# Performance work log

Measured on AMD Instinct MI355X. Metric: run time of the kernel, lower is better.

Reference implementation:

```python
import jax, jax.numpy as jnp
import numpy as np
from jax.scipy.ndimage import map_coordinates

H = 256          # detector height (pixels)
W = 256          # detector width (pixels)
PX = 1.6875      # pixel size (mm); W*PX = 432mm
PIERCE = 216.0   # piercing point offset (mm) -> centered detector
SAD = 742.5      # source-to-isocenter distance (mm)
DAD = 517.15     # detector-to-isocenter distance (mm)


def _rotmat(angles):
    # ZYX intrinsic Euler rotation from (alpha, beta, gamma)
    a, b, g = angles[0], angles[1], angles[2]
    ca, sa = jnp.cos(a), jnp.sin(a)
    cb, sb = jnp.cos(b), jnp.sin(b)
    cg, sg = jnp.cos(g), jnp.sin(g)
    Rz = jnp.array([[ca, -sa, 0.], [sa, ca, 0.], [0., 0., 1.]])
    Ry = jnp.array([[cb, 0., sb], [0., 1., 0.], [-sb, 0., cb]])
    Rx = jnp.array([[1., 0., 0.], [0., cg, -sg], [0., sg, cg]])
    return Rz @ Ry @ Rx


def setup_inputs() -> dict:
    key = jax.random.key(0)
    k1, k2 = jax.random.split(key)
    volume = jax.random.uniform(k1, (256, 256, 256), dtype=jnp.float32)  # CT attenuation
    batch = jax.random.normal(k2, (2, 6), dtype=jnp.float32) * 0.1       # [B, (rot3, trans3)]
    return {"volume": volume, "batch": batch, "n_samples": 256}


def reference(volume, batch, n_samples):
    B = batch.shape[0]
    center = jnp.asarray(volume.shape, dtype=volume.dtype) / 2.0  # volume center (mm, unit spacing)

    rots = batch[:, 0:3]
    trans = batch[:, 3:6]
    R = jax.vmap(_rotmat)(rots)                              # [B,3,3]
    iso = center[None, :] + trans                            # [B,3]

    z = jnp.array([0., 0., 1.], dtype=volume.dtype)
    source = iso + SAD * jnp.einsum('bij,j->bi', R, z)       # [B,3]
    det_c = iso - DAD * jnp.einsum('bij,j->bi', R, z)        # [B,3]
    u_ax = R[:, :, 0]                                        # detector u axis [B,3]
    v_ax = R[:, :, 1]                                        # detector v axis [B,3]

    us = (jnp.arange(W, dtype=volume.dtype) * PX - PIERCE)   # [W]
    vs = (jnp.arange(H, dtype=volume.dtype) * PX - PIERCE)   # [H]
    # target pixel positions on detector plane: [B,H,W,3]
    target = (det_c[:, None, None, :]
              + us[None, None, :, None] * u_ax[:, None, None, :]
              + vs[None, :, None, None] * v_ax[:, None, None, :])

    ray = target - source[:, None, None, :]                  # [B,H,W,3]
    length = jnp.linalg.norm(ray, axis=-1)                   # [B,H,W]

    t = jnp.linspace(0.0, 1.0, n_samples, dtype=volume.dtype)  # [S]
    # sample points along each ray: [B,S,H,W,3] (voxel coords, unit spacing)
    pts = source[:, None, None, None, :] + t[None, :, None, None, None] * ray[:, None, :, :, :]

    def sample_one(p):  # p: [S,H,W,3]
        return map_coordinates(volume, [p[..., 0], p[..., 1], p[..., 2]], order=1, mode='constant', cval=0.0)

    samples = jax.vmap(sample_one)(pts)                      # [B,S,H,W]
    img = samples.sum(axis=1) * (length / n_samples)         # line integral [B,H,W]

    img = img.reshape(B, -1)                                 # [B, H*W]
    mn = img.min(axis=1, keepdims=True)
    mx = img.max(axis=1, keepdims=True)
    img = (img - mn) / (mx - mn)
    img = 1.0 - img                                          # bone_dark=True
    return img.reshape(B, H, W)
```

## Files before the change

kernel.cpp:

```cpp
#include <hip/hip_runtime.h>
#include <hip/hip_fp16.h>


static __device__ __constant__ float kPX     = 1.6875f;
static __device__ __constant__ float kPIERCE = 216.0f;
static __device__ __constant__ float kSAD    = 742.5f;
static __device__ __constant__ float kDAD    = 517.15f;

#define VOL_BYTES   (256u * 256u * 256u * 4u)
#define PAIR_R      258u
#define PAIR_ELEMS  (256u * 256u * PAIR_R)
#define PAIR_BYTES  (PAIR_ELEMS * 4u)

__global__ void drr_init_mm(unsigned* mm) {
    int i = threadIdx.x;
    if (i < 4) mm[i] = (i & 1) ? 0u : 0x7F800000u;
}

__global__ __launch_bounds__(256) void drr_pack(const float* __restrict__ vol,
                                                __half2* __restrict__ vhp,
                                                unsigned* __restrict__ mm) {
    if (blockIdx.x == 0 && threadIdx.x < 4)
        mm[threadIdx.x] = (threadIdx.x & 1) ? 0u : 0x7F800000u;

    __shared__ float tile[65][65];
    const int bid  = blockIdx.x;
    const int y    = bid >> 4;
    const int t4   = bid & 15;
    const int x0   = (t4 & 3) << 6;
    const int z0   = (t4 >> 2) << 6;

    const int rr = threadIdx.x >> 4;
    const int cc = threadIdx.x & 15;
    #pragma unroll
    for (int base = 0; base < 80; base += 16) {
        const int r = base + rr;
        if (r < 65) {
            const int x = x0 - 1 + r;
            float4 f = make_float4(0.0f, 0.0f, 0.0f, 0.0f);
            if (x >= 0)
                f = *(const float4*)&vol[(x << 16) | (y << 8) | (z0 + (cc << 2))];
            tile[r][(cc << 2) + 0] = f.x;
            tile[r][(cc << 2) + 1] = f.y;
            tile[r][(cc << 2) + 2] = f.z;
            tile[r][(cc << 2) + 3] = f.w;
        }
    }
    __syncthreads();

    const int lane = threadIdx.x & 63;
    const int row4 = threadIdx.x >> 6;
    for (int r = row4; r < 64; r += 4) {
        const int z = z0 + r;
        const unsigned base = (unsigned)((z << 8) | y) * PAIR_R;
        vhp[base + x0 + lane] =
            __halves2half2(__float2half(tile[lane][r]), __float2half(tile[lane + 1][r]));
    }
    if ((t4 & 3) == 3) {
        for (int r = row4; r < 64; r += 4) {
            const int z = z0 + r;
            const unsigned base = (unsigned)((z << 8) | y) * PAIR_R;
            if (lane == 0) {
                vhp[base + 256] = __halves2half2(__float2half(tile[64][r]), __float2half(0.0f));
                vhp[base + 257] = __halves2half2(__float2half(0.0f), __float2half(0.0f));
            }
        }
    }
}

__device__ __forceinline__ void slab(float s, float r, float lo, float hi,
                                     float& tlo, float& thi) {
    if (fabsf(r) > 1e-8f) {
        const float inv = 1.0f / r;
        const float ta  = (lo - s) * inv;
        const float tb  = (hi - s) * inv;
        tlo = fmaxf(tlo, fminf(ta, tb));
        thi = fminf(thi, fmaxf(ta, tb));
    } else if (s < lo || s > hi) {
        tlo = 2.0f; thi = -1.0f;
    }
}

struct RayCfg {
    float rx, ry, rz, length;
    int k_lo, k_hi;
    int s_lo, s_hi;
};

__device__ __forceinline__ void cfg_windows(float sx, float sy, float sz, RayCfg& c) {
    float tlo = 0.0f, thi = 1.0f;
    slab(sx, c.rx, -1.02f, 256.02f, tlo, thi);
    slab(sy, c.ry, -1.02f, 256.02f, tlo, thi);
    slab(sz, c.rz, -1.02f, 256.02f, tlo, thi);
    c.k_lo = 0; c.k_hi = -1;
    if (thi >= tlo) {
        c.k_lo = max(0,   (int)ceilf(tlo * 255.0f - 1e-3f));
        c.k_hi = min(255, (int)floorf(thi * 255.0f + 1e-3f));
    }
    float slo = 0.0f, shi = 1.0f;
    slab(sx, c.rx, 0.01f, 254.99f, slo, shi);
    slab(sy, c.ry, 0.01f, 254.99f, slo, shi);
    slab(sz, c.rz, 0.01f, 254.99f, slo, shi);
    c.s_lo = 1; c.s_hi = -1;
    if (shi >= slo) {
        c.s_lo = (int)ceilf(slo * 255.0f + 1e-3f);
        c.s_hi = (int)floorf(shi * 255.0f - 1e-3f);
    }
}

__device__ __forceinline__ void ray_setup2(const float* __restrict__ batch,
                                           int b, int u, int v0,
                                           float& sx, float& sy, float& sz,
                                           RayCfg& A, RayCfg& B) {
    const float a  = batch[b * 6 + 0];
    const float be = batch[b * 6 + 1];
    const float g  = batch[b * 6 + 2];
    const float tx = batch[b * 6 + 3];
    const float ty = batch[b * 6 + 4];
    const float tz = batch[b * 6 + 5];

    float sa, ca, sb, cb, sg, cg;
    sincosf(a, &sa, &ca);
    sincosf(be, &sb, &cb);
    sincosf(g, &sg, &cg);

    const float R00 = ca * cb;
    const float R01 = ca * sb * sg - sa * cg;
    const float R02 = sa * sg + ca * sb * cg;
    const float R10 = sa * cb;
    const float R11 = ca * cg + sa * sb * sg;
    const float R12 = sa * sb * cg - ca * sg;
    const float R20 = -sb;
    const float R21 = cb * sg;
    const float R22 = cb * cg;

    sx = 128.0f + tx + kSAD * R02;
    sy = 128.0f + ty + kSAD * R12;
    sz = 128.0f + tz + kSAD * R22;

    const float uu = u * kPX - kPIERCE;
    const float vv = v0 * kPX - kPIERCE;
    A.rx = uu * R00 + vv * R01 - (kSAD + kDAD) * R02;
    A.ry = uu * R10 + vv * R11 - (kSAD + kDAD) * R12;
    A.rz = uu * R20 + vv * R21 - (kSAD + kDAD) * R22;
    B.rx = A.rx + kPX * R01;
    B.ry = A.ry + kPX * R11;
    B.rz = A.rz + kPX * R21;
    A.length = sqrtf(A.rx * A.rx + A.ry * A.ry + A.rz * A.rz);
    B.length = sqrtf(B.rx * B.rx + B.ry * B.ry + B.rz * B.rz);
    cfg_windows(sx, sy, sz, A);
    cfg_windows(sx, sy, sz, B);
}

__device__ __forceinline__ float tri_fast(const __half2* __restrict__ vhp,
                                          float sx, float sy, float sz,
                                          const RayCfg& c, float t) {
    const float px = fmaf(t, c.rx, sx);
    const float py = fmaf(t, c.ry, sy);
    const float pz = fmaf(t, c.rz, sz);
    const float fx = floorf(px), fy = floorf(py), fz = floorf(pz);
    const int ix = (int)fx, iy = (int)fy, iz = (int)fz;
    const float wx = px - fx, wy = py - fy, wz = pz - fz;

    const unsigned base = (unsigned)iz * 66048u + (unsigned)iy * 258u + (unsigned)(ix + 1);
    const __half2 q00 = vhp[base];
    const __half2 q01 = vhp[base + 66048u];
    const __half2 q10 = vhp[base + 258u];
    const __half2 q11 = vhp[base + 66306u];

    const float wx0 = 1.0f - wx, wy0 = 1.0f - wy, wz0 = 1.0f - wz;
    const float a00 = __low2float(q00) * wx0 + __high2float(q00) * wx;
    const float a01 = __low2float(q01) * wx0 + __high2float(q01) * wx;
    const float a10 = __low2float(q10) * wx0 + __high2float(q10) * wx;
    const float a11 = __low2float(q11) * wx0 + __high2float(q11) * wx;
    return (a00 * wz0 + a01 * wz) * wy0 + (a10 * wz0 + a11 * wz) * wy;
}

__device__ __forceinline__ float tri_slow(const __half2* __restrict__ vhp,
                                          float sx, float sy, float sz,
                                          const RayCfg& c, float t) {
    const float px = fmaf(t, c.rx, sx);
    const float py = fmaf(t, c.ry, sy);
    const float pz = fmaf(t, c.rz, sz);
    const float fx = floorf(px), fy = floorf(py), fz = floorf(pz);
    const int ix = (int)fx, iy = (int)fy, iz = (int)fz;
    const float wx = px - fx, wy = py - fy, wz = pz - fz;

    const float mx0 = ((unsigned)ix       < 256u) ? 1.0f : 0.0f;
    const float mx1 = ((unsigned)(ix + 1) < 256u) ? 1.0f : 0.0f;
    const float my0 = ((unsigned)iy       < 256u) ? 1.0f : 0.0f;
    const float my1 = ((unsigned)(iy + 1) < 256u) ? 1.0f : 0.0f;
    const float mz0 = ((unsigned)iz       < 256u) ? 1.0f : 0.0f;
    const float mz1 = ((unsigned)(iz + 1) < 256u) ? 1.0f : 0.0f;

    const int i  = min(max(ix + 1, 0), 257);
    const int y0 = min(max(iy,     0), 255);
    const int y1 = min(max(iy + 1, 0), 255);
    const int z0 = min(max(iz,     0), 255);
    const int z1 = min(max(iz + 1, 0), 255);

    const unsigned zt0 = (unsigned)z0 * 66048u;
    const unsigned zt1 = (unsigned)z1 * 66048u;
    const unsigned yt0 = (unsigned)y0 * 258u;
    const unsigned yt1 = (unsigned)y1 * 258u;

    const __half2 q00 = vhp[zt0 + yt0 + i];
    const __half2 q01 = vhp[zt1 + yt0 + i];
    const __half2 q10 = vhp[zt0 + yt1 + i];
    const __half2 q11 = vhp[zt1 + yt1 + i];

    const float wx0 = (1.0f - wx) * mx0, wx1 = wx * mx1;
    const float wy0 = (1.0f - wy) * my0, wy1 = wy * my1;
    const float wz0 = (1.0f - wz) * mz0, wz1 = wz * mz1;

    const float a00 = __low2float(q00) * wx0 + __high2float(q00) * wx1;
    const float a01 = __low2float(q01) * wx0 + __high2float(q01) * wx1;
    const float a10 = __low2float(q10) * wx0 + __high2float(q10) * wx1;
    const float a11 = __low2float(q11) * wx0 + __high2float(q11) * wx1;
    return (a00 * wz0 + a01 * wz1) * wy0 + (a10 * wz0 + a11 * wz1) * wy1;
}

__global__ __launch_bounds__(512, 4) void drr_main_pk2(const __half2* __restrict__ vhp,
                                                       const float* __restrict__ batch,
                                                       float* __restrict__ raw,
                                                       unsigned* __restrict__ mm) {
    const int tid  = threadIdx.x;
    const int lane = tid & 63;
    const int seg  = tid >> 6;

    const int blk = ((blockIdx.x & 7) << 7) | (blockIdx.x >> 3);
    const int b   = blk >> 9;
    const int ti  = blk & 511;
    const int u   = ((ti & 15) << 4) + (lane & 15);
    const int v0  = ((ti >> 4) << 3) + ((lane >> 4) << 1);

    float sx, sy, sz;
    RayCfg A, B;
    ray_setup2(batch, b, u, v0, sx, sy, sz, A, B);

    const int klo = min(A.k_lo, B.k_lo);
    const int khi = max(A.k_hi, B.k_hi);
    const int slo = max(A.s_lo, B.s_lo);
    const int shi = min(A.s_hi, B.s_hi);

    const float tstep = 1.0f / 255.0f;
    float sA = 0.0f, sB = 0.0f;
    for (int k = klo + seg; k <= khi; k += 8) {
        const float t = (float)k * tstep;
        if (k >= slo && k <= shi) {
            sA += tri_fast(vhp, sx, sy, sz, A, t);
            sB += tri_fast(vhp, sx, sy, sz, B, t);
        } else {
            sA += tri_slow(vhp, sx, sy, sz, A, t);
            sB += tri_slow(vhp, sx, sy, sz, B, t);
        }
    }

    __shared__ float pA[8][64], pB[8][64];
    pA[seg][lane] = sA;
    pB[seg][lane] = sB;
    __syncthreads();

    if (tid < 64) {
        float tA = 0.0f, tB = 0.0f;
        #pragma unroll
        for (int s = 0; s < 8; ++s) { tA += pA[s][lane]; tB += pB[s][lane]; }
        const float rA = tA * (A.length * (1.0f / 256.0f));
        const float rB = tB * (B.length * (1.0f / 256.0f));
        raw[(b << 16) + (v0 << 8) + u]       = rA;
        raw[(b << 16) + ((v0 + 1) << 8) + u] = rB;

        float mn = fminf(rA, rB), mx = fmaxf(rA, rB);
        #pragma unroll
        for (int off = 32; off >= 1; off >>= 1) {
            mn = fminf(mn, __shfl_xor(mn, off));
            mx = fmaxf(mx, __shfl_xor(mx, off));
        }
        if (lane == 0) {
            atomicMin(&mm[2 * b + 0], __float_as_uint(mn));
            atomicMax(&mm[2 * b + 1], __float_as_uint(mx));
        }
    }
}

__global__ __launch_bounds__(256) void drr_transpose(const float* __restrict__ vol,
                                                     float* __restrict__ volt) {
    __shared__ float tile[64][65];
    const int bid  = blockIdx.x;
    const int y    = bid >> 4;
    const int t4   = bid & 15;
    const int x0   = (t4 & 3) << 6;
    const int z0   = (t4 >> 2) << 6;
    const int lane = threadIdx.x & 63;
    const int row4 = threadIdx.x >> 6;

    #pragma unroll
    for (int i = 0; i < 16; ++i) {
        const int xr = (i << 2) + row4;
        tile[xr][lane] = vol[((x0 + xr) << 16) | (y << 8) | (z0 + lane)];
    }
    __syncthreads();
    #pragma unroll
    for (int i = 0; i < 16; ++i) {
        const int zr = (i << 2) + row4;
        volt[((z0 + zr) << 16) | (y << 8) | (x0 + lane)] = tile[lane][zr];
    }
}

__device__ __forceinline__ float tri_sample_f32(const float* __restrict__ vol,
                                                float sx, float sy, float sz,
                                                const RayCfg& c, float t) {
    const float px = fmaf(t, c.rx, sx);
    const float py = fmaf(t, c.ry, sy);
    const float pz = fmaf(t, c.rz, sz);
    const float fx = floorf(px), fy = floorf(py), fz = floorf(pz);
    const int ix = (int)fx, iy = (int)fy, iz = (int)fz;
    const float wx = px - fx, wy = py - fy, wz = pz - fz;
    const float mx0 = ((unsigned)ix       < 256u) ? 1.0f : 0.0f;
    const float mx1 = ((unsigned)(ix + 1) < 256u) ? 1.0f : 0.0f;
    const float my0 = ((unsigned)iy       < 256u) ? 1.0f : 0.0f;
    const float my1 = ((unsigned)(iy + 1) < 256u) ? 1.0f : 0.0f;
    const float mz0 = ((unsigned)iz       < 256u) ? 1.0f : 0.0f;
    const float mz1 = ((unsigned)(iz + 1) < 256u) ? 1.0f : 0.0f;
    const unsigned X0 = (unsigned)ix & 255u, X1 = (unsigned)(ix + 1) & 255u;
    const unsigned Y0 = ((unsigned)iy & 255u) << 8, Y1 = ((unsigned)(iy + 1) & 255u) << 8;
    const unsigned Z0 = ((unsigned)iz & 255u) << 16, Z1 = ((unsigned)(iz + 1) & 255u) << 16;
    const float v000 = vol[Z0 | Y0 | X0];
    const float v001 = vol[Z1 | Y0 | X0];
    const float v010 = vol[Z0 | Y1 | X0];
    const float v011 = vol[Z1 | Y1 | X0];
    const float v100 = vol[Z0 | Y0 | X1];
    const float v101 = vol[Z1 | Y0 | X1];
    const float v110 = vol[Z0 | Y1 | X1];
    const float v111 = vol[Z1 | Y1 | X1];
    const float wx0 = (1.0f - wx) * mx0, wx1 = wx * mx1;
    const float wy0 = (1.0f - wy) * my0, wy1 = wy * my1;
    const float wz0 = (1.0f - wz) * mz0, wz1 = wz * mz1;
    const float c00 = v000 * wz0 + v001 * wz1;
    const float c01 = v010 * wz0 + v011 * wz1;
    const float c10 = v100 * wz0 + v101 * wz1;
    const float c11 = v110 * wz0 + v111 * wz1;
    return (c00 * wy0 + c01 * wy1) * wx0 + (c10 * wy0 + c11 * wy1) * wx1;
}

__global__ __launch_bounds__(256, 4) void drr_main_f32(const float* __restrict__ volt,
                                                       const float* __restrict__ batch,
                                                       float* __restrict__ raw,
                                                       unsigned* __restrict__ mm) {
    const int tid  = threadIdx.x;
    const int lane = tid & 63;
    const int seg  = tid >> 6;
    const int tile = blockIdx.x;
    const int b    = tile >> 10;
    const int ti   = tile & 1023;
    const int u    = ((ti & 15) << 4) + (lane & 15);
    const int v    = ((ti >> 4) << 2) + (lane >> 4);

    float sx, sy, sz;
    RayCfg A, B;
    ray_setup2(batch, b, u, v, sx, sy, sz, A, B);

    const float tstep = 1.0f / 255.0f;
    float sum = 0.0f;
    for (int k = A.k_lo + seg; k <= A.k_hi; k += 4)
        sum += tri_sample_f32(volt, sx, sy, sz, A, (float)k * tstep);

    __shared__ float part[4][64];
    part[seg][lane] = sum;
    __syncthreads();

    if (tid < 64) {
        const float s = part[0][lane] + part[1][lane] + part[2][lane] + part[3][lane];
        const float rawv = s * (A.length * (1.0f / 256.0f));
        raw[(b << 16) + (v << 8) + u] = rawv;
        float mn = rawv, mx = rawv;
        #pragma unroll
        for (int off = 32; off >= 1; off >>= 1) {
            mn = fminf(mn, __shfl_xor(mn, off));
            mx = fmaxf(mx, __shfl_xor(mx, off));
        }
        if (lane == 0) {
            atomicMin(&mm[2 * b + 0], __float_as_uint(mn));
            atomicMax(&mm[2 * b + 1], __float_as_uint(mx));
        }
    }
}

__global__ __launch_bounds__(256) void drr_norm(float* __restrict__ img,
                                                const unsigned* __restrict__ mm) {
    const int gid = blockIdx.x * 256 + threadIdx.x;
    const int b   = gid >> 16;
    const float mn  = __uint_as_float(mm[2 * b + 0]);
    const float mx  = __uint_as_float(mm[2 * b + 1]);
    const float inv = 1.0f / (mx - mn);
    img[gid] = 1.0f - (img[gid] - mn) * inv;
}

extern "C" void kernel_launch(void* const* d_in, const int* in_sizes, int n_in,
                              void* d_out, int out_size, void* d_ws, size_t ws_size,
                              hipStream_t stream) {
    const float* vol   = (const float*)d_in[0];
    const float* batch = (const float*)d_in[1];
    float* out         = (float*)d_out;

    if (ws_size >= (size_t)PAIR_BYTES + 16) {
        __half2*  vhp = (__half2*)d_ws;
        unsigned* mm  = (unsigned*)((char*)d_ws + PAIR_BYTES);
        drr_pack<<<4096, 256, 0, stream>>>(vol, vhp, mm);
        drr_main_pk2<<<1024, 512, 0, stream>>>(vhp, batch, out, mm);
        drr_norm<<<512, 256, 0, stream>>>(out, mm);
    } else {
        float*    volt = (float*)d_ws;
        unsigned* mm   = (unsigned*)((char*)d_ws + VOL_BYTES);
        drr_init_mm<<<1, 64, 0, stream>>>(mm);
        drr_transpose<<<4096, 256, 0, stream>>>(vol, volt);
        drr_main_f32<<<2048, 256, 0, stream>>>(volt, batch, out, mm);
        drr_norm<<<512, 256, 0, stream>>>(out, mm);
    }
}
```

Measured before the change: 95.13 us.

## Split ray samples across four blocks with atomic accumulation and separate min/max pass

The main ray-marching kernel now splits each tile's sample range across four 256-thread blocks (4096 blocks in total) instead of one 512-thread block per tile. Partial line integrals are combined with float atomicAdd into an output that the pack kernel zeroes first. Because per-pixel sums are only final once all blocks finish, the min/max reduction moves into a new kernel launched before normalisation. The half-precision pack also switches to a packed round-toward-zero conversion intrinsic. In exchange this adds atomics, an extra launch and nondeterministic summation order.

```diff
diff --git a/kernel.cpp b/kernel.cpp
--- a/kernel.cpp
+++ b/kernel.cpp
@@ -12,6 +12,13 @@
 #define PAIR_ELEMS  (256u * 256u * PAIR_R)
 #define PAIR_BYTES  (PAIR_ELEMS * 4u)
 
+typedef __fp16 half2_raw __attribute__((ext_vector_type(2)));
+
+__device__ __forceinline__ __half2 pack_h2(float lo, float hi) {
+    half2_raw h = __builtin_amdgcn_cvt_pkrtz(lo, hi);
+    return __builtin_bit_cast(__half2, h);
+}
+
 __global__ void drr_init_mm(unsigned* mm) {
     int i = threadIdx.x;
     if (i < 4) mm[i] = (i & 1) ? 0u : 0x7F800000u;
@@ -19,12 +26,15 @@
 
 __global__ __launch_bounds__(256) void drr_pack(const float* __restrict__ vol,
                                                 __half2* __restrict__ vhp,
+                                                float* __restrict__ raw,
                                                 unsigned* __restrict__ mm) {
-    if (blockIdx.x == 0 && threadIdx.x < 4)
+    const int bid = blockIdx.x;
+    if (bid == 0 && threadIdx.x < 4)
         mm[threadIdx.x] = (threadIdx.x & 1) ? 0u : 0x7F800000u;
+    if (threadIdx.x < 32)
+        raw[(bid << 5) + threadIdx.x] = 0.0f;
 
     __shared__ float tile[65][65];
-    const int bid  = blockIdx.x;
     const int y    = bid >> 4;
     const int t4   = bid & 15;
     const int x0   = (t4 & 3) << 6;
@@ -53,16 +63,15 @@
     for (int r = row4; r < 64; r += 4) {
         const int z = z0 + r;
         const unsigned base = (unsigned)((z << 8) | y) * PAIR_R;
-        vhp[base + x0 + lane] =
-            __halves2half2(__float2half(tile[lane][r]), __float2half(tile[lane + 1][r]));
+        vhp[base + x0 + lane] = pack_h2(tile[lane][r], tile[lane + 1][r]);
     }
     if ((t4 & 3) == 3) {
         for (int r = row4; r < 64; r += 4) {
             const int z = z0 + r;
             const unsigned base = (unsigned)((z << 8) | y) * PAIR_R;
             if (lane == 0) {
-                vhp[base + 256] = __halves2half2(__float2half(tile[64][r]), __float2half(0.0f));
-                vhp[base + 257] = __halves2half2(__float2half(0.0f), __float2half(0.0f));
+                vhp[base + 256] = pack_h2(tile[64][r], 0.0f);
+                vhp[base + 257] = pack_h2(0.0f, 0.0f);
             }
         }
     }
@@ -220,19 +229,19 @@
     return (a00 * wz0 + a01 * wz1) * wy0 + (a10 * wz0 + a11 * wz1) * wy1;
 }
 
-__global__ __launch_bounds__(512, 4) void drr_main_pk2(const __half2* __restrict__ vhp,
+__global__ __launch_bounds__(256, 8) void drr_main_pk3(const __half2* __restrict__ vhp,
                                                        const float* __restrict__ batch,
-                                                       float* __restrict__ raw,
-                                                       unsigned* __restrict__ mm) {
+                                                       float* __restrict__ raw) {
     const int tid  = threadIdx.x;
     const int lane = tid & 63;
     const int seg  = tid >> 6;
 
-    const int blk = ((blockIdx.x & 7) << 7) | (blockIdx.x >> 3);
-    const int b   = blk >> 9;
-    const int ti  = blk & 511;
-    const int u   = ((ti & 15) << 4) + (lane & 15);
-    const int v0  = ((ti >> 4) << 3) + ((lane >> 4) << 1);
+    const int kq   = blockIdx.x & 3;
+    const int tile = blockIdx.x >> 2;
+    const int b    = tile >> 9;
+    const int ti   = tile & 511;
+    const int u    = ((ti & 15) << 4) + (lane & 15);
+    const int v0   = ((ti >> 4) << 3) + ((lane >> 4) << 1);
 
     float sx, sy, sz;
     RayCfg A, B;
@@ -245,7 +254,7 @@
 
     const float tstep = 1.0f / 255.0f;
     float sA = 0.0f, sB = 0.0f;
-    for (int k = klo + seg; k <= khi; k += 8) {
+    for (int k = klo + (kq << 2) + seg; k <= khi; k += 16) {
         const float t = (float)k * tstep;
         if (k >= slo && k <= shi) {
             sA += tri_fast(vhp, sx, sy, sz, A, t);
@@ -256,31 +265,46 @@
         }
     }
 
-    __shared__ float pA[8][64], pB[8][64];
+    __shared__ float pA[4][64], pB[4][64];
     pA[seg][lane] = sA;
     pB[seg][lane] = sB;
     __syncthreads();
 
     if (tid < 64) {
-        float tA = 0.0f, tB = 0.0f;
-        #pragma unroll
-        for (int s = 0; s < 8; ++s) { tA += pA[s][lane]; tB += pB[s][lane]; }
-        const float rA = tA * (A.length * (1.0f / 256.0f));
-        const float rB = tB * (B.length * (1.0f / 256.0f));
-        raw[(b << 16) + (v0 << 8) + u]       = rA;
-        raw[(b << 16) + ((v0 + 1) << 8) + u] = rB;
-
-        float mn = fminf(rA, rB), mx = fmaxf(rA, rB);
-        #pragma unroll
-        for (int off = 32; off >= 1; off >>= 1) {
-            mn = fminf(mn, __shfl_xor(mn, off));
-            mx = fmaxf(mx, __shfl_xor(mx, off));
-        }
-        if (lane == 0) {
-            atomicMin(&mm[2 * b + 0], __float_as_uint(mn));
-            atomicMax(&mm[2 * b + 1], __float_as_uint(mx));
-        }
-    }
+        const float tA = pA[0][lane] + pA[1][lane] + pA[2][lane] + pA[3][lane];
+        const float tB = pB[0][lane] + pB[1][lane] + pB[2][lane] + pB[3][lane];
+        if (tA != 0.0f)
+            atomicAdd(&raw[(b << 16) + (v0 << 8) + u],       tA * (A.length * (1.0f / 256.0f)));
+        if (tB != 0.0f)
+            atomicAdd(&raw[(b << 16) + ((v0 + 1) << 8) + u], tB * (B.length * (1.0f / 256.0f)));
+    }
+}
+
+__global__ __launch_bounds__(256) void drr_minmax(const float* __restrict__ raw,
+                                                  unsigned* __restrict__ mm) {
+    const int gid = blockIdx.x * 256 + threadIdx.x;
+    const int b   = gid >> 16;
+    const float x = raw[gid];
+    float mn = x, mx = x;
+    #pragma unroll
+    for (int off = 32; off >= 1; off >>= 1) {
+        mn = fminf(mn, __shfl_xor(mn, off));
+        mx = fmaxf(mx, __shfl_xor(mx, off));
+    }
+    if ((threadIdx.x & 63) == 0) {
+        atomicMin(&mm[2 * b + 0], __float_as_uint(mn));
+        atomicMax(&mm[2 * b + 1], __float_as_uint(mx));
+    }
+}
+
+__global__ __launch_bounds__(256) void drr_norm(float* __restrict__ img,
+                                                const unsigned* __restrict__ mm) {
+    const int gid = blockIdx.x * 256 + threadIdx.x;
+    const int b   = gid >> 16;
+    const float mn  = __uint_as_float(mm[2 * b + 0]);
+    const float mx  = __uint_as_float(mm[2 * b + 1]);
+    const float inv = 1.0f / (mx - mn);
+    img[gid] = 1.0f - (img[gid] - mn) * inv;
 }
 
 __global__ __launch_bounds__(256) void drr_transpose(const float* __restrict__ vol,
@@ -386,16 +410,6 @@
     }
 }
 
-__global__ __launch_bounds__(256) void drr_norm(float* __restrict__ img,
-                                                const unsigned* __restrict__ mm) {
-    const int gid = blockIdx.x * 256 + threadIdx.x;
-    const int b   = gid >> 16;
-    const float mn  = __uint_as_float(mm[2 * b + 0]);
-    const float mx  = __uint_as_float(mm[2 * b + 1]);
-    const float inv = 1.0f / (mx - mn);
-    img[gid] = 1.0f - (img[gid] - mn) * inv;
-}
-
 extern "C" void kernel_launch(void* const* d_in, const int* in_sizes, int n_in,
                               void* d_out, int out_size, void* d_ws, size_t ws_size,
                               hipStream_t stream) {
@@ -406,8 +420,9 @@
     if (ws_size >= (size_t)PAIR_BYTES + 16) {
         __half2*  vhp = (__half2*)d_ws;
         unsigned* mm  = (unsigned*)((char*)d_ws + PAIR_BYTES);
-        drr_pack<<<4096, 256, 0, stream>>>(vol, vhp, mm);
-        drr_main_pk2<<<1024, 512, 0, stream>>>(vhp, batch, out, mm);
+        drr_pack<<<4096, 256, 0, stream>>>(vol, vhp, out, mm);
+        drr_main_pk3<<<4096, 256, 0, stream>>>(vhp, batch, out);
+        drr_minmax<<<512, 256, 0, stream>>>(out, mm);
         drr_norm<<<512, 256, 0, stream>>>(out, mm);
     } else {
         float*    volt = (float*)d_ws;
```

Result: slower. 128.4 us (+34.9%).
